# Kernel tuning notes

Measured on AMD Instinct MI355X. Metric: run time of the kernel, lower is better.

The kernel has to match this reference:

```python
import jax, jax.numpy as jnp
import numpy as np

N_NODES = 100000
N_EDGES = 3200000
IN_DIM = 20
HID = 64


def setup_inputs() -> dict:
    key = jax.random.key(0)
    ks = jax.random.split(key, 8)
    x = jax.random.normal(ks[0], (N_NODES, IN_DIM), dtype=jnp.float32)
    edge_index = jax.random.randint(ks[1], (2, N_EDGES), 0, N_NODES, dtype=jnp.int64)
    # SAGEConv layer 1: lin_l (neighbor agg, with bias), lin_r (root, no bias)
    s1 = 1.0 / np.sqrt(IN_DIM)
    W1l = jax.random.uniform(ks[2], (IN_DIM, HID), minval=-s1, maxval=s1, dtype=jnp.float32)
    b1 = jnp.zeros((HID,), dtype=jnp.float32)
    W1r = jax.random.uniform(ks[3], (IN_DIM, HID), minval=-s1, maxval=s1, dtype=jnp.float32)
    # SAGEConv layer 2
    s2 = 1.0 / np.sqrt(HID)
    W2l = jax.random.uniform(ks[4], (HID, HID), minval=-s2, maxval=s2, dtype=jnp.float32)
    b2 = jnp.zeros((HID,), dtype=jnp.float32)
    W2r = jax.random.uniform(ks[5], (HID, HID), minval=-s2, maxval=s2, dtype=jnp.float32)
    return {"x": x, "edge_index": edge_index, "W1l": W1l, "b1": b1, "W1r": W1r,
            "W2l": W2l, "b2": b2, "W2r": W2r}


def _sage_conv(x, src, dst, deg_inv, Wl, bl, Wr, n_nodes):
    # mean-aggregate source-node features into target nodes
    msg = x[src]  # [E, d] gather
    agg = jax.ops.segment_sum(msg, dst, num_segments=n_nodes)  # [N, d]
    agg = agg * deg_inv[:, None]
    return agg @ Wl + bl + x @ Wr


def reference(x, edge_index, W1l, b1, W1r, W2l, b2, W2r):
    src = edge_index[0]
    dst = edge_index[1]
    n = x.shape[0]
    ones = jnp.ones((src.shape[0],), dtype=x.dtype)
    deg = jax.ops.segment_sum(ones, dst, num_segments=n)  # in-degree
    deg_inv = jnp.where(deg > 0, 1.0 / jnp.maximum(deg, 1.0), 0.0)
    h = jax.nn.relu(_sage_conv(x, src, dst, deg_inv, W1l, b1, W1r, n))
    h = _sage_conv(h, src, dst, deg_inv, W2l, b2, W2r, n)
    return h.mean(axis=0)  # [HID]
```

## Files before the change

kernel.cpp:

```cpp
#include <hip/hip_runtime.h>
#include <hip/hip_bf16.h>

#define N_NODES 100000
#define N_EDGES 3200000
#define IN_DIM 20
#define HID 64
#define SCAN_CHUNK 1024

__global__ void k_detect(const unsigned* __restrict__ e, int* __restrict__ flag)
{
    int lane = threadIdx.x;
    unsigned hi = e[2 * lane + 1];
    unsigned long long ballot = __ballot(hi != 0u);
    if (lane == 0) *flag = (ballot == 0ULL) ? 1 : 0;
}

__device__ __forceinline__ void load_edge(const void* eidx, int i64, int e, int E,
                                          int& s, int& d)
{
    if (i64) {
        const long long* p = (const long long*)eidx;
        s = (int)p[e];
        d = (int)p[(long)E + e];
    } else {
        const int* p = (const int*)eidx;
        s = p[e];
        d = p[(long)E + e];
    }
}

__global__ __launch_bounds__(256) void k_hist(
    const void* __restrict__ eidx, const int* __restrict__ flag,
    int* __restrict__ cnt, int E, int N)
{
    const int i64 = *flag;
    int stride = gridDim.x * blockDim.x;
    for (int e = blockIdx.x * blockDim.x + threadIdx.x; e < E; e += stride) {
        int d;
        if (i64) d = (int)((const long long*)eidx)[(long)E + e];
        else     d = ((const int*)eidx)[(long)E + e];
        if ((unsigned)d < (unsigned)N) atomicAdd(&cnt[d], 1);
    }
}

__global__ __launch_bounds__(SCAN_CHUNK) void k_scan_block(
    const int* __restrict__ cnt, int* __restrict__ offs, int* __restrict__ bsum, int N)
{
    __shared__ int buf[2][SCAN_CHUNK];
    int t = threadIdx.x;
    int gid = blockIdx.x * SCAN_CHUNK + t;
    int v = (gid < N) ? cnt[gid] : 0;
    int cur = 0;
    buf[0][t] = v;
    __syncthreads();
    for (int off = 1; off < SCAN_CHUNK; off <<= 1) {
        int nv = buf[cur][t] + ((t >= off) ? buf[cur][t - off] : 0);
        buf[cur ^ 1][t] = nv;
        cur ^= 1;
        __syncthreads();
    }
    int inc = buf[cur][t];
    if (gid < N) offs[gid] = inc - v;
    if (t == SCAN_CHUNK - 1) bsum[blockIdx.x] = inc;
}

__global__ void k_scan_partials(int* __restrict__ bsum, int nb)
{
    if (threadIdx.x == 0) {
        int run = 0;
        for (int b = 0; b < nb; ++b) { int v = bsum[b]; bsum[b] = run; run += v; }
    }
}

__global__ __launch_bounds__(256) void k_scan_add(
    int* __restrict__ offs, int* __restrict__ cursor, float* __restrict__ deginv,
    const int* __restrict__ cnt, const int* __restrict__ bsum, int N)
{
    int i = blockIdx.x * blockDim.x + threadIdx.x;
    if (i < N) {
        int o = offs[i] + bsum[i >> 10];
        offs[i] = o;
        cursor[i] = o;
        int c = cnt[i];
        deginv[i] = (c > 0) ? 1.0f / (float)c : 0.0f;
    }
}

__global__ __launch_bounds__(256) void k_scatter(
    const void* __restrict__ eidx, const int* __restrict__ flag,
    int* __restrict__ cursor, int* __restrict__ csr,
    const float* __restrict__ deginv, float* __restrict__ w, int E, int N)
{
    const int i64 = *flag;
    int stride = gridDim.x * blockDim.x;
    for (int e = blockIdx.x * blockDim.x + threadIdx.x; e < E; e += stride) {
        int s, d;
        load_edge(eidx, i64, e, E, s, d);
        if ((unsigned)s >= (unsigned)N || (unsigned)d >= (unsigned)N) continue;
        int pos = atomicAdd(&cursor[d], 1);
        csr[pos] = s;
        atomicAdd(&w[s], deginv[d]);
    }
}

__global__ __launch_bounds__(256) void k_agg(
    const int* __restrict__ offs, const int* __restrict__ cnt,
    const int* __restrict__ csr, const float* __restrict__ x,
    float* __restrict__ agg1, int N)
{
    const int lane = threadIdx.x & 63;
    const int wid = (blockIdx.x * blockDim.x + threadIdx.x) >> 6;
    const int wtot = (gridDim.x * blockDim.x) >> 6;
    const int g = lane / 20;
    const int dim = lane % 20;
    const bool active = lane < 60;

    for (int n = wid; n < N; n += wtot) {
        int base = offs[n];
        int c = cnt[n];
        float v = 0.0f;
        if (active) {
            for (int i = g; i < c; i += 3) {
                int s = csr[base + i];
                v += x[(long)s * IN_DIM + dim];
            }
        }
        float v1 = __shfl(v, lane + 20);
        float v2 = __shfl(v, lane + 40);
        if (lane < 20) agg1[(long)n * IN_DIM + lane] = v + v1 + v2;
    }
}

__global__ __launch_bounds__(256) void k_node_layer1(
    const float* __restrict__ x, const float* __restrict__ agg1,
    const float* __restrict__ deginv, const float* __restrict__ w,
    const float* __restrict__ W1l, const float* __restrict__ b1,
    const float* __restrict__ W1r,
    float* __restrict__ S1, float* __restrict__ S2, int N)
{
    __shared__ float sW1l[IN_DIM * HID];
    __shared__ float sW1r[IN_DIM * HID];
    __shared__ float sb1[HID];
    for (int i = threadIdx.x; i < IN_DIM * HID; i += blockDim.x) {
        sW1l[i] = W1l[i];
        sW1r[i] = W1r[i];
    }
    if (threadIdx.x < HID) sb1[threadIdx.x] = b1[threadIdx.x];
    __syncthreads();

    const int lane = threadIdx.x & 63;
    const int wave_id = (blockIdx.x * blockDim.x + threadIdx.x) >> 6;
    const int waves_total = (gridDim.x * blockDim.x) >> 6;

    float s1 = 0.0f, s2 = 0.0f;
    for (int n = wave_id; n < N; n += waves_total) {
        float v = 0.0f;
        if (lane < IN_DIM) v = agg1[(long)n * IN_DIM + lane];
        else if (lane >= 32 && lane < 32 + IN_DIM) v = x[(long)n * IN_DIM + (lane - 32)];
        float di = deginv[n];
        float h = sb1[lane];
        #pragma unroll
        for (int k = 0; k < IN_DIM; ++k) {
            float ak = __shfl(v, k) * di;
            float xk = __shfl(v, 32 + k);
            h += ak * sW1l[k * HID + lane];
            h += xk * sW1r[k * HID + lane];
        }
        h = fmaxf(h, 0.0f);
        s2 += h;
        s1 += w[n] * h;
    }
    atomicAdd(&S1[lane], s1);
    atomicAdd(&S2[lane], s2);
}

__global__ void k_final(const float* __restrict__ S1, const float* __restrict__ S2,
                        const float* __restrict__ W2l, const float* __restrict__ b2,
                        const float* __restrict__ W2r, float* __restrict__ out, float invN)
{
    int j = threadIdx.x;
    float acc1 = 0.0f, acc2 = 0.0f;
    for (int k = 0; k < HID; ++k) {
        acc1 += S1[k] * W2l[k * HID + j];
        acc2 += S2[k] * W2r[k * HID + j];
    }
    out[j] = acc1 * invN + b2[j] + acc2 * invN;
}

__global__ __launch_bounds__(256) void k_edge_agg_atomic(
    const void* __restrict__ eidx, const int* __restrict__ flag,
    const float* __restrict__ x, float* __restrict__ agg1, int E, int N)
{
    const int i64 = *flag;
    int stride = gridDim.x * blockDim.x;
    for (int e = blockIdx.x * blockDim.x + threadIdx.x; e < E; e += stride) {
        int s, d;
        load_edge(eidx, i64, e, E, s, d);
        if ((unsigned)s >= (unsigned)N || (unsigned)d >= (unsigned)N) continue;
        const float* xs = x + (long)s * IN_DIM;
        float* ad = agg1 + (long)d * IN_DIM;
        #pragma unroll
        for (int k = 0; k < IN_DIM; ++k) atomicAdd(&ad[k], xs[k]);
    }
}

__global__ __launch_bounds__(256) void k_edge_w(
    const void* __restrict__ eidx, const int* __restrict__ flag,
    const float* __restrict__ deginv, float* __restrict__ w, int E, int N)
{
    const int i64 = *flag;
    int stride = gridDim.x * blockDim.x;
    for (int e = blockIdx.x * blockDim.x + threadIdx.x; e < E; e += stride) {
        int s, d;
        load_edge(eidx, i64, e, E, s, d);
        if ((unsigned)s >= (unsigned)N || (unsigned)d >= (unsigned)N) continue;
        atomicAdd(&w[s], deginv[d]);
    }
}

__global__ __launch_bounds__(256) void k_deginv_from_cnt(
    const int* __restrict__ cnt, float* __restrict__ deginv, int N)
{
    int i = blockIdx.x * blockDim.x + threadIdx.x;
    if (i < N) {
        int c = cnt[i];
        deginv[i] = (c > 0) ? 1.0f / (float)c : 0.0f;
    }
}

extern "C" void kernel_launch(void* const* d_in, const int* in_sizes, int n_in,
                              void* d_out, int out_size, void* d_ws, size_t ws_size,
                              hipStream_t stream)
{
    const float* x   = (const float*)d_in[0];
    const void* eidx = (const void*)d_in[1];
    const float* W1l = (const float*)d_in[2];
    const float* b1  = (const float*)d_in[3];
    const float* W1r = (const float*)d_in[4];
    const float* W2l = (const float*)d_in[5];
    const float* b2  = (const float*)d_in[6];
    const float* W2r = (const float*)d_in[7];
    float* out = (float*)d_out;

    const int N = N_NODES;
    const int E = N_EDGES;
    const long NL = N;

    const size_t words_needed = 25 * (size_t)N + (size_t)E + 64 + 64 + 1 + 128;

    int*   cnt    = (int*)d_ws;
    float* wvec   = (float*)d_ws + NL;
    float* deginv = (float*)d_ws + 2 * NL;
    int*   offs   = (int*)d_ws + 3 * NL;
    int*   cursor = (int*)d_ws + 4 * NL;
    int*   csr    = (int*)d_ws + 5 * NL;
    float* agg1   = (float*)d_ws + 5 * NL + E;
    float* S1     = (float*)d_ws + 25 * NL + E;
    float* S2     = S1 + HID;
    int*   flag   = (int*)(S2 + HID);
    int*   bsum   = flag + 1;

    if (ws_size >= words_needed * 4) {
        hipMemsetAsync(d_ws, 0, 2 * (size_t)N * sizeof(int), stream);
        hipMemsetAsync(S1, 0, (2 * HID + 1) * sizeof(float), stream);

        k_detect<<<1, 64, 0, stream>>>((const unsigned*)eidx, flag);
        k_hist<<<2048, 256, 0, stream>>>(eidx, flag, cnt, E, N);

        int nb = (N + SCAN_CHUNK - 1) / SCAN_CHUNK;
        k_scan_block<<<nb, SCAN_CHUNK, 0, stream>>>(cnt, offs, bsum, N);
        k_scan_partials<<<1, 64, 0, stream>>>(bsum, nb);
        k_scan_add<<<(N + 255) / 256, 256, 0, stream>>>(offs, cursor, deginv, cnt, bsum, N);

        k_scatter<<<2048, 256, 0, stream>>>(eidx, flag, cursor, csr, deginv, wvec, E, N);
        k_agg<<<1024, 256, 0, stream>>>(offs, cnt, csr, x, agg1, N);
        k_node_layer1<<<256, 256, 0, stream>>>(x, agg1, deginv, wvec, W1l, b1, W1r, S1, S2, N);
        k_final<<<1, HID, 0, stream>>>(S1, S2, W2l, b2, W2r, out, 1.0f / (float)N);
    } else {
        float* agg1f = (float*)d_ws + 3 * NL;
        float* S1f   = (float*)d_ws + 23 * NL;
        float* S2f   = S1f + HID;
        int*   flagf = (int*)(S2f + HID);

        hipMemsetAsync(d_ws, 0, (23 * (size_t)N + 2 * HID + 1) * sizeof(float), stream);
        k_detect<<<1, 64, 0, stream>>>((const unsigned*)eidx, flagf);
        k_hist<<<2048, 256, 0, stream>>>(eidx, flagf, cnt, E, N);
        k_deginv_from_cnt<<<(N + 255) / 256, 256, 0, stream>>>(cnt, deginv, N);
        k_edge_agg_atomic<<<2048, 256, 0, stream>>>(eidx, flagf, x, agg1f, E, N);
        k_edge_w<<<2048, 256, 0, stream>>>(eidx, flagf, deginv, wvec, E, N);
        k_node_layer1<<<256, 256, 0, stream>>>(x, agg1f, deginv, wvec, W1l, b1, W1r, S1f, S2f, N);
        k_final<<<1, HID, 0, stream>>>(S1f, S2f, W2l, b2, W2r, out, 1.0f / (float)N);
    }
}
```

Baseline: 827.5 us.

## Replace CSR scan with fixed-capacity per-node buckets and gather-based layer 2

```diff
diff --git a/kernel.cpp b/kernel.cpp
--- a/kernel.cpp
+++ b/kernel.cpp
@@ -5,6 +5,8 @@
 #define N_EDGES 3200000
 #define IN_DIM 20
 #define HID 64
+#define CAP 96
+#define SPILL_CAP 8192
 #define SCAN_CHUNK 1024
 
 __global__ void k_detect(const unsigned* __restrict__ e, int* __restrict__ flag)
@@ -29,17 +31,39 @@
     }
 }
 
-__global__ __launch_bounds__(256) void k_hist(
+__global__ __launch_bounds__(256) void k_bucket(
     const void* __restrict__ eidx, const int* __restrict__ flag,
-    int* __restrict__ cnt, int E, int N)
+    int* __restrict__ cnt, int* __restrict__ bucket,
+    float* __restrict__ spill_agg, const float* __restrict__ x,
+    int* __restrict__ spill_cnt, int* __restrict__ spill_list, int E, int N)
 {
     const int i64 = *flag;
     int stride = gridDim.x * blockDim.x;
     for (int e = blockIdx.x * blockDim.x + threadIdx.x; e < E; e += stride) {
-        int d;
-        if (i64) d = (int)((const long long*)eidx)[(long)E + e];
-        else     d = ((const int*)eidx)[(long)E + e];
-        if ((unsigned)d < (unsigned)N) atomicAdd(&cnt[d], 1);
+        int s, d;
+        load_edge(eidx, i64, e, E, s, d);
+        if ((unsigned)s >= (unsigned)N || (unsigned)d >= (unsigned)N) continue;
+        int pos = atomicAdd(&cnt[d], 1);
+        if (pos < CAP) {
+            bucket[(long)d * CAP + pos] = s;
+        } else {
+            const float* xs = x + (long)s * IN_DIM;
+            float* sa = spill_agg + (long)d * IN_DIM;
+            #pragma unroll
+            for (int k = 0; k < IN_DIM; ++k) atomicAdd(&sa[k], xs[k]);
+            int sp = atomicAdd(spill_cnt, 1);
+            if (sp < SPILL_CAP) { spill_list[2 * sp] = d; spill_list[2 * sp + 1] = s; }
+        }
+    }
+}
+
+__global__ __launch_bounds__(256) void k_deginv_from_cnt(
+    const int* __restrict__ cnt, float* __restrict__ deginv, int N)
+{
+    int i = blockIdx.x * blockDim.x + threadIdx.x;
+    if (i < N) {
+        int c = cnt[i];
+        deginv[i] = (c > 0) ? 1.0f / (float)c : 0.0f;
     }
 }
 
@@ -86,7 +110,139 @@
     }
 }
 
-__global__ __launch_bounds__(256) void k_scatter(
+__global__ __launch_bounds__(256) void k_scatter_nw(
+    const void* __restrict__ eidx, const int* __restrict__ flag,
+    int* __restrict__ cursor, int* __restrict__ csr, int E, int N)
+{
+    const int i64 = *flag;
+    int stride = gridDim.x * blockDim.x;
+    for (int e = blockIdx.x * blockDim.x + threadIdx.x; e < E; e += stride) {
+        int s, d;
+        load_edge(eidx, i64, e, E, s, d);
+        if ((unsigned)s >= (unsigned)N || (unsigned)d >= (unsigned)N) continue;
+        int pos = atomicAdd(&cursor[d], 1);
+        csr[pos] = s;
+    }
+}
+
+__global__ __launch_bounds__(256) void k_fused1(
+    const int* __restrict__ cursor_or_null, const int* __restrict__ cnt,
+    const int* __restrict__ list, const float* __restrict__ x,
+    const float* __restrict__ deginv, const float* __restrict__ spill_agg,
+    const float* __restrict__ W1l, const float* __restrict__ b1,
+    const float* __restrict__ W1r,
+    float* __restrict__ h, float* __restrict__ S2, int N)
+{
+    __shared__ float sW1l[IN_DIM * HID];
+    __shared__ float sW1r[IN_DIM * HID];
+    __shared__ float sb1[HID];
+    for (int i = threadIdx.x; i < IN_DIM * HID; i += blockDim.x) {
+        sW1l[i] = W1l[i];
+        sW1r[i] = W1r[i];
+    }
+    if (threadIdx.x < HID) sb1[threadIdx.x] = b1[threadIdx.x];
+    __syncthreads();
+
+    const int lane = threadIdx.x & 63;
+    const int wid = (blockIdx.x * blockDim.x + threadIdx.x) >> 6;
+    const int wtot = (gridDim.x * blockDim.x) >> 6;
+    const int g = lane / 20;
+    const int dim = lane % 20;
+    const bool active = lane < 60;
+
+    float s2 = 0.0f;
+    for (int n = wid; n < N; n += wtot) {
+        int c = cnt[n];
+        int limit = cursor_or_null ? c : min(c, CAP);
+        long base = cursor_or_null ? (long)cursor_or_null[n] - c : (long)n * CAP;
+        float v = 0.0f;
+        if (active) {
+            for (int i = g; i < limit; i += 3) {
+                int s = list[base + i];
+                v += x[(long)s * IN_DIM + dim];
+            }
+        }
+        float v1 = __shfl(v, lane + 20);
+        float v2 = __shfl(v, lane + 40);
+        float va = 0.0f;
+        if (lane < IN_DIM) va = v + v1 + v2 + spill_agg[(long)n * IN_DIM + lane];
+        float xr = 0.0f;
+        if (lane >= 32 && lane < 32 + IN_DIM) xr = x[(long)n * IN_DIM + (lane - 32)];
+        float di = deginv[n];
+        float hh = sb1[lane];
+        #pragma unroll
+        for (int k = 0; k < IN_DIM; ++k) {
+            float ak = __shfl(va, k) * di;
+            float xk = __shfl(xr, 32 + k);
+            hh += ak * sW1l[k * HID + lane] + xk * sW1r[k * HID + lane];
+        }
+        hh = fmaxf(hh, 0.0f);
+        h[(long)n * HID + lane] = hh;
+        s2 += hh;
+    }
+    atomicAdd(&S2[lane], s2);
+}
+
+__global__ __launch_bounds__(256) void k_gather2(
+    const int* __restrict__ cursor_or_null, const int* __restrict__ cnt,
+    const int* __restrict__ list, const float* __restrict__ deginv,
+    const float* __restrict__ h, const int* __restrict__ spill_cnt,
+    const int* __restrict__ spill_list, float* __restrict__ S1, int N)
+{
+    const int lane = threadIdx.x & 63;
+    const int wid = (blockIdx.x * blockDim.x + threadIdx.x) >> 6;
+    const int wtot = (gridDim.x * blockDim.x) >> 6;
+
+    float s1 = 0.0f;
+    for (int n = wid; n < N; n += wtot) {
+        int c = cnt[n];
+        int limit = cursor_or_null ? c : min(c, CAP);
+        long base = cursor_or_null ? (long)cursor_or_null[n] - c : (long)n * CAP;
+        float hs = 0.0f;
+        for (int i = 0; i < limit; ++i) {
+            int s = list[base + i];
+            hs += h[(long)s * HID + lane];
+        }
+        s1 += deginv[n] * hs;
+    }
+    if (wid == 0) {
+        int nsp = min(*spill_cnt, SPILL_CAP);
+        for (int i = 0; i < nsp; ++i) {
+            int d = spill_list[2 * i], s = spill_list[2 * i + 1];
+            s1 += deginv[d] * h[(long)s * HID + lane];
+        }
+    }
+    atomicAdd(&S1[lane], s1);
+}
+
+__global__ void k_final(const float* __restrict__ S1, const float* __restrict__ S2,
+                        const float* __restrict__ W2l, const float* __restrict__ b2,
+                        const float* __restrict__ W2r, float* __restrict__ out, float invN)
+{
+    int j = threadIdx.x;
+    float acc1 = 0.0f, acc2 = 0.0f;
+    for (int k = 0; k < HID; ++k) {
+        acc1 += S1[k] * W2l[k * HID + j];
+        acc2 += S2[k] * W2r[k * HID + j];
+    }
+    out[j] = acc1 * invN + b2[j] + acc2 * invN;
+}
+
+__global__ __launch_bounds__(256) void k_hist(
+    const void* __restrict__ eidx, const int* __restrict__ flag,
+    int* __restrict__ cnt, int E, int N)
+{
+    const int i64 = *flag;
+    int stride = gridDim.x * blockDim.x;
+    for (int e = blockIdx.x * blockDim.x + threadIdx.x; e < E; e += stride) {
+        int d;
+        if (i64) d = (int)((const long long*)eidx)[(long)E + e];
+        else     d = ((const int*)eidx)[(long)E + e];
+        if ((unsigned)d < (unsigned)N) atomicAdd(&cnt[d], 1);
+    }
+}
+
+__global__ __launch_bounds__(256) void k_scatter_w(
     const void* __restrict__ eidx, const int* __restrict__ flag,
     int* __restrict__ cursor, int* __restrict__ csr,
     const float* __restrict__ deginv, float* __restrict__ w, int E, int N)
@@ -174,60 +330,6 @@
     atomicAdd(&S2[lane], s2);
 }
 
-__global__ void k_final(const float* __restrict__ S1, const float* __restrict__ S2,
-                        const float* __restrict__ W2l, const float* __restrict__ b2,
-                        const float* __restrict__ W2r, float* __restrict__ out, float invN)
-{
-    int j = threadIdx.x;
-    float acc1 = 0.0f, acc2 = 0.0f;
-    for (int k = 0; k < HID; ++k) {
-        acc1 += S1[k] * W2l[k * HID + j];
-        acc2 += S2[k] * W2r[k * HID + j];
-    }
-    out[j] = acc1 * invN + b2[j] + acc2 * invN;
-}
-
-__global__ __launch_bounds__(256) void k_edge_agg_atomic(
-    const void* __restrict__ eidx, const int* __restrict__ flag,
-    const float* __restrict__ x, float* __restrict__ agg1, int E, int N)
-{
-    const int i64 = *flag;
-    int stride = gridDim.x * blockDim.x;
-    for (int e = blockIdx.x * blockDim.x + threadIdx.x; e < E; e += stride) {
-        int s, d;
-        load_edge(eidx, i64, e, E, s, d);
-        if ((unsigned)s >= (unsigned)N || (unsigned)d >= (unsigned)N) continue;
-        const float* xs = x + (long)s * IN_DIM;
-        float* ad = agg1 + (long)d * IN_DIM;
-        #pragma unroll
-        for (int k = 0; k < IN_DIM; ++k) atomicAdd(&ad[k], xs[k]);
-    }
-}
-
-__global__ __launch_bounds__(256) void k_edge_w(
-    const void* __restrict__ eidx, const int* __restrict__ flag,
-    const float* __restrict__ deginv, float* __restrict__ w, int E, int N)
-{
-    const int i64 = *flag;
-    int stride = gridDim.x * blockDim.x;
-    for (int e = blockIdx.x * blockDim.x + threadIdx.x; e < E; e += stride) {
-        int s, d;
-        load_edge(eidx, i64, e, E, s, d);
-        if ((unsigned)s >= (unsigned)N || (unsigned)d >= (unsigned)N) continue;
-        atomicAdd(&w[s], deginv[d]);
-    }
-}
-
-__global__ __launch_bounds__(256) void k_deginv_from_cnt(
-    const int* __restrict__ cnt, float* __restrict__ deginv, int N)
-{
-    int i = blockIdx.x * blockDim.x + threadIdx.x;
-    if (i < N) {
-        int c = cnt[i];
-        deginv[i] = (c > 0) ? 1.0f / (float)c : 0.0f;
-    }
-}
-
 extern "C" void kernel_launch(void* const* d_in, const int* in_sizes, int n_in,
                               void* d_out, int out_size, void* d_ws, size_t ws_size,
                               hipStream_t stream)
@@ -246,49 +348,83 @@
     const int E = N_EDGES;
     const long NL = N;
 
-    const size_t words_needed = 25 * (size_t)N + (size_t)E + 64 + 64 + 1 + 128;
+    const size_t tail_words = 64 + 64 + 1 + 1 + 2 * SPILL_CAP + 128;
+    const size_t words_H  = 182UL * N + tail_words;
+    const size_t words_Hp = 120UL * N + tail_words;
 
     int*   cnt    = (int*)d_ws;
-    float* wvec   = (float*)d_ws + NL;
-    float* deginv = (float*)d_ws + 2 * NL;
-    int*   offs   = (int*)d_ws + 3 * NL;
-    int*   cursor = (int*)d_ws + 4 * NL;
-    int*   csr    = (int*)d_ws + 5 * NL;
-    float* agg1   = (float*)d_ws + 5 * NL + E;
-    float* S1     = (float*)d_ws + 25 * NL + E;
-    float* S2     = S1 + HID;
-    int*   flag   = (int*)(S2 + HID);
-    int*   bsum   = flag + 1;
-
-    if (ws_size >= words_needed * 4) {
-        hipMemsetAsync(d_ws, 0, 2 * (size_t)N * sizeof(int), stream);
-        hipMemsetAsync(S1, 0, (2 * HID + 1) * sizeof(float), stream);
+    float* deginv = (float*)d_ws + NL;
+    float* spagg  = (float*)d_ws + 2 * NL;
+    float* h      = (float*)d_ws + 22 * NL;
+
+    if (ws_size >= words_H * 4) {
+        int* bucket = (int*)d_ws + 86 * NL;
+        float* S1   = (float*)d_ws + 182 * NL;
+        float* S2   = S1 + HID;
+        int* flag   = (int*)(S2 + HID);
+        int* spcnt  = flag + 1;
+        int* splist = spcnt + 1;
+
+        hipMemsetAsync(d_ws, 0, 22 * (size_t)N * sizeof(int), stream);
+        hipMemsetAsync(S1, 0, (2 * HID + 2) * sizeof(float), stream);
+
+        k_detect<<<1, 64, 0, stream>>>((const unsigned*)eidx, flag);
+        k_bucket<<<2048, 256, 0, stream>>>(eidx, flag, cnt, bucket, spagg, x, spcnt, splist, E, N);
+        k_deginv_from_cnt<<<(N + 255) / 256, 256, 0, stream>>>(cnt, deginv, N);
+        k_fused1<<<1024, 256, 0, stream>>>(nullptr, cnt, bucket, x, deginv, spagg,
+                                           W1l, b1, W1r, h, S2, N);
+        k_gather2<<<1024, 256, 0, stream>>>(nullptr, cnt, bucket, deginv, h, spcnt, splist, S1, N);
+        k_final<<<1, HID, 0, stream>>>(S1, S2, W2l, b2, W2r, out, 1.0f / (float)N);
+    } else if (ws_size >= words_Hp * 4) {
+        int* csr    = (int*)d_ws + 86 * NL;
+        int* offs   = (int*)d_ws + 118 * NL;
+        int* cursor = (int*)d_ws + 119 * NL;
+        float* S1   = (float*)d_ws + 120 * NL;
+        float* S2   = S1 + HID;
+        int* flag   = (int*)(S2 + HID);
+        int* spcnt  = flag + 1;
+        int* splist = spcnt + 1;
+        int* bsum   = splist + 2 * SPILL_CAP;
+
+        hipMemsetAsync(d_ws, 0, 22 * (size_t)N * sizeof(int), stream);
+        hipMemsetAsync(S1, 0, (2 * HID + 2) * sizeof(float), stream);
 
         k_detect<<<1, 64, 0, stream>>>((const unsigned*)eidx, flag);
         k_hist<<<2048, 256, 0, stream>>>(eidx, flag, cnt, E, N);
-
         int nb = (N + SCAN_CHUNK - 1) / SCAN_CHUNK;
         k_scan_block<<<nb, SCAN_CHUNK, 0, stream>>>(cnt, offs, bsum, N);
         k_scan_partials<<<1, 64, 0, stream>>>(bsum, nb);
         k_scan_add<<<(N + 255) / 256, 256, 0, stream>>>(offs, cursor, deginv, cnt, bsum, N);
-
-        k_scatter<<<2048, 256, 0, stream>>>(eidx, flag, cursor, csr, deginv, wvec, E, N);
-        k_agg<<<1024, 256, 0, stream>>>(offs, cnt, csr, x, agg1, N);
-        k_node_layer1<<<256, 256, 0, stream>>>(x, agg1, deginv, wvec, W1l, b1, W1r, S1, S2, N);
+        k_scatter_nw<<<2048, 256, 0, stream>>>(eidx, flag, cursor, csr, E, N);
+        k_fused1<<<1024, 256, 0, stream>>>(cursor, cnt, csr, x, deginv, spagg,
+                                           W1l, b1, W1r, h, S2, N);
+        k_gather2<<<1024, 256, 0, stream>>>(cursor, cnt, csr, deginv, h, spcnt, splist, S1, N);
         k_final<<<1, HID, 0, stream>>>(S1, S2, W2l, b2, W2r, out, 1.0f / (float)N);
     } else {
-        float* agg1f = (float*)d_ws + 3 * NL;
-        float* S1f   = (float*)d_ws + 23 * NL;
-        float* S2f   = S1f + HID;
-        int*   flagf = (int*)(S2f + HID);
-
-        hipMemsetAsync(d_ws, 0, (23 * (size_t)N + 2 * HID + 1) * sizeof(float), stream);
-        k_detect<<<1, 64, 0, stream>>>((const unsigned*)eidx, flagf);
-        k_hist<<<2048, 256, 0, stream>>>(eidx, flagf, cnt, E, N);
-        k_deginv_from_cnt<<<(N + 255) / 256, 256, 0, stream>>>(cnt, deginv, N);
-        k_edge_agg_atomic<<<2048, 256, 0, stream>>>(eidx, flagf, x, agg1f, E, N);
-        k_edge_w<<<2048, 256, 0, stream>>>(eidx, flagf, deginv, wvec, E, N);
-        k_node_layer1<<<256, 256, 0, stream>>>(x, agg1f, deginv, wvec, W1l, b1, W1r, S1f, S2f, N);
-        k_final<<<1, HID, 0, stream>>>(S1f, S2f, W2l, b2, W2r, out, 1.0f / (float)N);
-    }
-}
+        int*   cntL    = (int*)d_ws;
+        float* wvec    = (float*)d_ws + NL;
+        float* deginvL = (float*)d_ws + 2 * NL;
+        int*   offs    = (int*)d_ws + 3 * NL;
+        int*   cursor  = (int*)d_ws + 4 * NL;
+        int*   csr     = (int*)d_ws + 5 * NL;
+        float* agg1    = (float*)d_ws + 5 * NL + E;
+        float* S1      = (float*)d_ws + 25 * NL + E;
+        float* S2      = S1 + HID;
+        int*   flag    = (int*)(S2 + HID);
+        int*   bsum    = flag + 1;
+
+        hipMemsetAsync(d_ws, 0, 2 * (size_t)N * sizeof(int), stream);
+        hipMemsetAsync(S1, 0, (2 * HID + 1) * sizeof(float), stream);
+
+        k_detect<<<1, 64, 0, stream>>>((const unsigned*)eidx, flag);
+        k_hist<<<2048, 256, 0, stream>>>(eidx, flag, cntL, E, N);
+        int nb = (N + SCAN_CHUNK - 1) / SCAN_CHUNK;
+        k_scan_block<<<nb, SCAN_CHUNK, 0, stream>>>(cntL, offs, bsum, N);
+        k_scan_partials<<<1, 64, 0, stream>>>(bsum, nb);
+        k_scan_add<<<(N + 255) / 256, 256, 0, stream>>>(offs, cursor, deginvL, cntL, bsum, N);
+        k_scatter_w<<<2048, 256, 0, stream>>>(eidx, flag, cursor, csr, deginvL, wvec, E, N);
+        k_agg<<<1024, 256, 0, stream>>>(offs, cntL, csr, x, agg1, N);
+        k_node_layer1<<<256, 256, 0, stream>>>(x, agg1, deginvL, wvec, W1l, b1, W1r, S1, S2, N);
+        k_final<<<1, HID, 0, stream>>>(S1, S2, W2l, b2, W2r, out, 1.0f / (float)N);
+    }
+}
```

Result: slower. 1.121 ms (+35.4%).
